# Kernel tuning notes

Hardware: AMD Instinct MI355X
Metric: run time of the kernel (lower is better)

## Reference

```python
import jax, jax.numpy as jnp
import numpy as np

DIM = 192
HEADS = 4
CH = DIM // HEADS          # 48 channels per head
HID = int(DIM * 2.66)      # 510
EPS = 1e-5


def _dwconv(x, w):
    # depthwise 3x3, x: [b,c,h,w], w: [c,1,3,3]
    return jax.lax.conv_general_dilated(
        x, w, window_strides=(1, 1), padding='SAME',
        feature_group_count=x.shape[1],
        dimension_numbers=('NCHW', 'OIHW', 'NCHW'))


def _conv1x1(w, x):
    # w: [out,in], x: [b,in,h,w]
    return jnp.einsum('oc,bchw->bohw', w, x)


def _chan_ln(x, w, b):
    # LayerNorm over channel dim (equivalent to to_3d -> LN(last) -> to_4d)
    mu = jnp.mean(x, axis=1, keepdims=True)
    var = jnp.mean((x - mu) ** 2, axis=1, keepdims=True)
    return (x - mu) / jnp.sqrt(var + EPS) * w[None, :, None, None] + b[None, :, None, None]


def _l2norm(x):
    n = jnp.sqrt(jnp.sum(x * x, axis=-1, keepdims=True))
    return x / jnp.maximum(n, 1e-12)


def setup_inputs() -> dict:
    key = jax.random.key(0)
    ks = jax.random.split(key, 12)
    s = 0.02
    inp = {
        'lr': jax.random.normal(ks[0], (2, DIM, 128, 128), jnp.float32),
        'ref': jax.random.normal(ks[1], (2, DIM, 128, 128), jnp.float32),
        'ln1_w': jnp.ones((DIM,), jnp.float32), 'ln1_b': jnp.zeros((DIM,), jnp.float32),
        'lnr_w': jnp.ones((DIM,), jnp.float32), 'lnr_b': jnp.zeros((DIM,), jnp.float32),
        'ln2_w': jnp.ones((DIM,), jnp.float32), 'ln2_b': jnp.zeros((DIM,), jnp.float32),
        'Wq': jax.random.normal(ks[2], (DIM, DIM), jnp.float32) * s,
        'q_dw': jax.random.normal(ks[3], (DIM, 1, 3, 3), jnp.float32) * s,
        'Wkv': jax.random.normal(ks[4], (2 * DIM, DIM), jnp.float32) * s,
        'kv_dw': jax.random.normal(ks[5], (2 * DIM, 1, 3, 3), jnp.float32) * s,
        'Wproj': jax.random.normal(ks[6], (DIM, DIM), jnp.float32) * s,
        'Wca': jax.random.normal(ks[7], (2 * CH, CH), jnp.float32) * s,
        'temperature': jnp.ones((HEADS, 1, 1), jnp.float32),
        'Wpin': jax.random.normal(ks[8], (2 * HID, DIM), jnp.float32) * s,
        'ffn_dw': jax.random.normal(ks[9], (2 * HID, 1, 3, 3), jnp.float32) * s,
        'Wpout': jax.random.normal(ks[10], (DIM, HID), jnp.float32) * s,
    }
    return inp


def reference(lr, ref, ln1_w, ln1_b, lnr_w, lnr_b, ln2_w, ln2_b,
              Wq, q_dw, Wkv, kv_dw, Wproj, Wca, temperature,
              Wpin, ffn_dw, Wpout):
    b, c, h, w = lr.shape
    L = h * w

    lr_ln = _chan_ln(lr, ln1_w, ln1_b)
    ref_ln = _chan_ln(ref, lnr_w, lnr_b)

    # ---- channel cross-attention ----
    q = _dwconv(_conv1x1(Wq, lr_ln), q_dw)            # [b,c,h,w]
    kv = _dwconv(_conv1x1(Wkv, ref_ln), kv_dw)        # [b,2c,h,w]
    k, v = jnp.split(kv, 2, axis=1)

    q = _l2norm(q.reshape(b, HEADS, CH, L))           # [b,H,ch,L]
    k = _l2norm(k.reshape(b, HEADS, CH, L))
    v = v.reshape(b, HEADS, CH, L)

    attn = jnp.einsum('bhcl,bhdl->bhcd', q, k) * temperature[None]  # [b,H,ch,ch]
    attn0 = jax.nn.softmax(attn, axis=-1)

    a1 = jnp.maximum(attn, 0.0) ** 2
    a1 = jax.nn.gelu(a1, approximate=False) * a1
    # att_ca: 1x1 conv over the last (column) axis of attn1
    x_att = jnp.einsum('oj,bhij->bhio', Wca, a1)      # [b,H,ch,2*ch]
    scale, shift = jnp.split(x_att, 2, axis=-1)
    attn = attn0 * (1.0 + scale) + shift

    out = jnp.einsum('bhcd,bhdl->bhcl', attn, v).reshape(b, c, h, w)
    out = _conv1x1(Wproj, out)
    lr = lr + out

    # ---- GDFN ----
    x = _conv1x1(Wpin, _chan_ln(lr, ln2_w, ln2_b))    # [b,2*HID,h,w]
    x1, x2 = jnp.split(_dwconv(x, ffn_dw), 2, axis=1)
    x = jax.nn.gelu(x1, approximate=False) * x2
    x = _conv1x1(Wpout, x)
    return lr + x
```

## Files before the change

### kernel.cpp

```cpp
#include <hip/hip_runtime.h>
#include <hip/hip_bf16.h>
#include <math.h>

#define L     16384
#define IMG   128
#define BATCH 2
#define C0    192
#define NH    4
#define CHN   48
#define HID   510
#define HID2  1020
#define BL    (BATCH*L)
#define KSPL  128

typedef float  f32x4  __attribute__((ext_vector_type(4)));
typedef __bf16 bf16x8 __attribute__((ext_vector_type(8)));

union UB16 { uint4 u; bf16x8 v; };

__device__ __forceinline__ bf16x8 ld_bf8(const ushort* p){ UB16 x; x.u = *(const uint4*)p; return x.v; }
__device__ __forceinline__ f32x4 mfma16(bf16x8 a, bf16x8 b, f32x4 c){
  return __builtin_amdgcn_mfma_f32_16x16x32_bf16(a, b, c, 0, 0, 0);
}
__device__ __forceinline__ float u2f(ushort u){ union{unsigned u; float f;} x; x.u = ((unsigned)u)<<16; return x.f; }
__device__ __forceinline__ ushort f2u(float f){ __hip_bfloat16 h = __float2bfloat16(f); return *reinterpret_cast<ushort*>(&h); }
__device__ __forceinline__ float gelu_exact(float x){ return 0.5f*x*(1.0f+erff(x*0.70710678118654752f)); }

__global__ __launch_bounds__(256) void ln_stats3_k(const float* __restrict__ x0, const float* __restrict__ x1,
                                                   float* __restrict__ mu0, float* __restrict__ rs0,
                                                   float* __restrict__ mu1, float* __restrict__ rs1,
                                                   ushort* __restrict__ xf0, ushort* __restrict__ xf1){
  int z = blockIdx.y;
  const float* x = z ? x1 : x0;
  float* mu = z ? mu1 : mu0;
  float* rsig = z ? rs1 : rs0;
  ushort* xf = z ? xf1 : xf0;
  int pos = blockIdx.x*256 + threadIdx.x;
  int b = pos >> 14, l = pos & (L-1);
  const float* xp = x + (size_t)b*C0*L + l;
  ushort* base = xf + (size_t)b*C0*L;
  int pt = l >> 4, c16 = l & 15;
  float s=0.f, ss=0.f;
  #pragma unroll
  for (int st=0; st<6; ++st)
    #pragma unroll
    for (int g=0; g<4; ++g){
      ushort u8[8];
      #pragma unroll
      for (int j=0;j<8;++j){
        float v = xp[(size_t)(st*32 + g*8 + j)*L];
        s += v; ss += v*v; u8[j] = f2u(v);
      }
      *(uint4*)(base + ((size_t)(pt*6+st)*64 + g*16 + c16)*8) = *(const uint4*)u8;
    }
  float m = s*(1.f/C0);
  float var = ss*(1.f/C0) - m*m;
  mu[pos]=m; rsig[pos]=rsqrtf(var + 1e-5f);
}

__global__ void finln_k(const float* __restrict__ sum, const float* __restrict__ ss,
                        float* __restrict__ mu, float* __restrict__ rs){
  int i = blockIdx.x*256 + threadIdx.x;
  float m = sum[i]*(1.f/C0);
  float v = ss[i]*(1.f/C0) - m*m;
  mu[i] = m; rs[i] = rsqrtf(v + 1e-5f);
}

__device__ __forceinline__ void packwf_body(const float* __restrict__ W, const float* __restrict__ lnw,
                                            ushort* __restrict__ out, int Csrc, int O, int KS,
                                            int idx, int total){
  if (idx >= total) return;
  int j = idx & 7; int t = idx >> 3;
  int lane = t & 63; t >>= 6;
  int st = t % KS; int mt = t / KS;
  int m = mt*16 + (lane & 15);
  int k = st*32 + (lane >> 4)*8 + j;
  float v = 0.f;
  if (m < O && k < Csrc){ v = W[(size_t)m*Csrc + k]; if (lnw) v *= lnw[k]; }
  out[idx] = f2u(v);
}
__device__ __forceinline__ void prepab_body(const float* __restrict__ W, const float* __restrict__ lnw,
                                            const float* __restrict__ lnb, float* __restrict__ A,
                                            float* __restrict__ Bv, int Cc, int O, int Opad, int o){
  if (o >= Opad) return;
  float a=0.f,b=0.f;
  if (o < O){
    const float* wr = W + (size_t)o*Cc;
    for (int c=0;c<Cc;++c){ float w=wr[c]; a = fmaf(w, lnw[c], a); b = fmaf(w, lnb[c], b); }
  }
  A[o]=a; Bv[o]=b;
}

__global__ void prep_all_k(const float* Wq, const float* ln1w, const float* ln1b, ushort* Aqf, float* Aqv, float* Bqv,
                           const float* Wkv, const float* lnrw, const float* lnrb, ushort* Akvf, float* Akvv, float* Bkvv,
                           const float* Wpin, const float* ln2w, const float* ln2b, ushort* Apinf, float* Apinv, float* Bpinv,
                           const float* Wpout, ushort* Apoutf){
  int bx = blockIdx.x, tid = threadIdx.x;
  if (bx < 144)        packwf_body(Wq,   ln1w, Aqf,   192, 192, 6,  bx*256+tid,        36864);
  else if (bx < 432)   packwf_body(Wkv,  lnrw, Akvf,  192, 384, 6,  (bx-144)*256+tid,  73728);
  else if (bx < 1200)  packwf_body(Wpin, ln2w, Apinf, 192, 1020, 6, (bx-432)*256+tid,  196608);
  else if (bx < 1584)  packwf_body(Wpout, nullptr, Apoutf, 510, 192, 16, (bx-1200)*256+tid, 98304);
  else if (bx == 1584) prepab_body(Wq,  ln1w, ln1b, Aqv,  Bqv,  192, 192, 192,  tid);
  else if (bx < 1587)  prepab_body(Wkv, lnrw, lnrb, Akvv, Bkvv, 192, 384, 384,  (bx-1585)*256+tid);
  else                 prepab_body(Wpin,ln2w, ln2b, Apinv,Bpinv,192, 1020, 1024,(bx-1587)*256+tid);
}

template<int EPI, int WR, int KS, int BN>
__global__ __launch_bounds__(256, WR==2?3:4) void gemm5_k(
    const ushort* __restrict__ Af, int aBS,
    const ushort* __restrict__ Xf, size_t xBS,
    const float* __restrict__ mu, const float* __restrict__ rs,
    const float* __restrict__ Avec, const float* __restrict__ Bvec,
    const float* __restrict__ res,
    void* __restrict__ outp, int Orows, int Ovalid,
    ushort* __restrict__ outf, float* __restrict__ sum_acc, float* __restrict__ ss_acc)
{
  constexpr int BM  = WR*64;
  constexpr int NF  = (WR==2) ? 4 : (BN/64);
  constexpr int PB  = L/BN;
  constexpr int BLD = BN+8;
  constexpr int NSH = (EPI==0)? BM*BLD : (EPI==3 ? BN*72 : 64);
  __shared__ ushort bb[NSH];

  const int tid=threadIdx.x, lane=tid&63, w=tid>>6;
  const int g16=lane>>4, c16=lane&15;
  const int cpx = gridDim.x>>3;
  const int p = (blockIdx.x&7)*cpx + (blockIdx.x>>3);
  const int b = p / PB;
  const int l0 = (p - b*PB)*BN;
  const int mbase = blockIdx.y*BM;
  const int wr = (WR==2)? (w>>1)*64 : 0;
  const int wc = (WR==2)? (w&1)*64 : w*(BN/4);
  const int mt0 = (mbase+wr)>>4;
  const int pt0 = (l0+wc)>>4;

  const ushort* Ap = Af + (size_t)b*aBS + ((size_t)(mt0*KS)*64 + lane)*8;
  const ushort* Bp = Xf + (size_t)b*xBS + ((size_t)(pt0*KS)*64 + lane)*8;

  f32x4 acc[4][NF];
  #pragma unroll
  for (int mi=0;mi<4;++mi)
    #pragma unroll
    for (int ni=0;ni<NF;++ni){ f32x4 z={0.f,0.f,0.f,0.f}; acc[mi][ni]=z; }

  bf16x8 ar[2][4], br[2][NF];
  #pragma unroll
  for (int i=0;i<4;++i) ar[0][i] = ld_bf8(Ap + (size_t)(i*KS)*512);
  #pragma unroll
  for (int i=0;i<NF;++i) br[0][i] = ld_bf8(Bp + (size_t)(i*KS)*512);
  #pragma unroll
  for (int st=0; st<KS; ++st){
    const int cur = st&1, nxt = cur^1;
    if (st+1 < KS){
      #pragma unroll
      for (int i=0;i<4;++i)  ar[nxt][i] = ld_bf8(Ap + (size_t)(i*KS + st+1)*512);
      #pragma unroll
      for (int i=0;i<NF;++i) br[nxt][i] = ld_bf8(Bp + (size_t)(i*KS + st+1)*512);
    }
    #pragma unroll
    for (int mi=0;mi<4;++mi)
      #pragma unroll
      for (int ni=0;ni<NF;++ni)
        acc[mi][ni] = mfma16(ar[cur][mi], br[cur][ni], acc[mi][ni]);
  }

  if (EPI==0){
    #pragma unroll
    for (int ni=0;ni<NF;++ni){
      int nl = wc + ni*16 + c16;
      int posl = b*L + l0 + nl;
      float muv = mu[posl], rsv = rs[posl];
      #pragma unroll
      for (int mi=0;mi<4;++mi)
        #pragma unroll
        for (int r=0;r<4;++r){
          int ro = wr + mi*16 + g16*4 + r;
          int o  = mbase + ro;
          bb[ro*BLD + nl] = f2u(rsv*(acc[mi][ni][r] - muv*Avec[o]) + Bvec[o]);
        }
    }
    __syncthreads();
    constexpr int SEG = BN/64;
    constexpr int JOBS = BM*SEG;
    if (tid < JOBS){
      int row = tid/SEG, seg = tid%SEG;
      if (mbase + row < Ovalid){
        ushort* dst = (ushort*)outp + ((size_t)b*Orows + mbase + row)*L + l0 + seg*64;
        const ushort* src = &bb[row*BLD + seg*64];
        #pragma unroll
        for (int i=0;i<8;++i) *(uint4*)(dst + i*8) = *(const uint4*)(src + i*8);
      }
    }
  } else if (EPI==3){
    #pragma unroll
    for (int ni=0;ni<NF;++ni){
      int nl = wc + ni*16 + c16;
      int posl = b*L + l0 + nl;
      size_t cbase = ((size_t)b*Orows + mbase)*L + l0 + nl;
      float s1=0.f, s2=0.f;
      #pragma unroll
      for (int mi=0;mi<4;++mi)
        #pragma unroll
        for (int r=0;r<4;++r){
          int ro = mi*16 + g16*4 + r;
          size_t idx = cbase + (size_t)ro*L;
          float v = res[idx] + acc[mi][ni][r];
          ((float*)outp)[idx] = v;
          s1 += v; s2 += v*v;
          bb[nl*72 + ro] = f2u(v);
        }
      s1 += __shfl_xor(s1,16,64); s1 += __shfl_xor(s1,32,64);
      s2 += __shfl_xor(s2,16,64); s2 += __shfl_xor(s2,32,64);
      if (g16==0){ atomicAdd(&sum_acc[posl], s1); atomicAdd(&ss_acc[posl], s2); }
    }
    __syncthreads();
    constexpr int PTS = BN/16;
    int ph  = tid >> 7;
    int rm  = tid & 127;
    int stl = rm >> 6;
    int gf  = (rm >> 4) & 3;
    int cf  = rm & 15;
    int stg = (mbase >> 5) + stl;
    #pragma unroll
    for (int pp=0; pp<PTS/2; ++pp){
      int ptl = ph*(PTS/2) + pp;
      int nl  = ptl*16 + cf;
      uint4 v = *(const uint4*)&bb[nl*72 + stl*32 + gf*8];
      int ptg = (l0 >> 4) + ptl;
      *(uint4*)(outf + (size_t)b*C0*L + ((size_t)(ptg*6 + stg)*64 + gf*16 + cf)*8) = v;
    }
  } else {
    #pragma unroll
    for (int ni=0;ni<NF;++ni){
      int nl = wc + ni*16 + c16;
      #pragma unroll
      for (int mi=0;mi<4;++mi)
        #pragma unroll
        for (int r=0;r<4;++r){
          int o = mbase + wr + mi*16 + g16*4 + r;
          size_t idx = ((size_t)b*Orows + o)*L + l0 + nl;
          ((float*)outp)[idx] += acc[mi][ni][r];
        }
    }
  }
}

__global__ __launch_bounds__(256) void dwconvQK_k(const ushort* __restrict__ qpre, const ushort* __restrict__ kvpre,
    const float* __restrict__ qdw, const float* __restrict__ kvdw,
    ushort* __restrict__ qb, ushort* __restrict__ kb,
    float* __restrict__ qss, float* __restrict__ kss){
  int bx = blockIdx.x;
  bool isK = bx >= 3072;
  const ushort* in = isK ? kvpre : qpre;
  size_t inBS = isK ? (size_t)384*L : (size_t)192*L;
  const float* w9 = isK ? kvdw : qdw;
  ushort* out = isK ? kb : qb;
  float* ss = isK ? kss : qss;
  int e  = (isK ? bx-3072 : bx)*256 + threadIdx.x;
  int bc = e >> 11;
  int p  = (e & 2047) * 8;
  int c  = bc % 192, b = bc / 192;
  int y  = p >> 7, x0 = p & 127;
  const ushort* ip = in + (size_t)b*inBS + (size_t)c*L;
  float w[9];
  #pragma unroll
  for (int i=0;i<9;++i) w[i] = w9[c*9+i];
  float v[3][10];
  #pragma unroll
  for (int r=0;r<3;++r){
    int yy = y + r - 1;
    if ((unsigned)yy >= IMG){
      #pragma unroll
      for (int j=0;j<10;++j) v[r][j]=0.f;
    } else {
      const ushort* rp = ip + yy*IMG + x0;
      uint4 cv = *(const uint4*)rp; const ushort* us = (const ushort*)&cv;
      #pragma unroll
      for (int j=0;j<8;++j) v[r][j+1] = u2f(us[j]);
      v[r][0] = (x0>0)   ? u2f(rp[-1]) : 0.f;
      v[r][9] = (x0<120) ? u2f(rp[8])  : 0.f;
    }
  }
  float sq = 0.f; ushort o8[8];
  #pragma unroll
  for (int j=0;j<8;++j){
    float a = 0.f;
    #pragma unroll
    for (int r=0;r<3;++r)
      #pragma unroll
      for (int dx=0;dx<3;++dx) a = fmaf(w[r*3+dx], v[r][j+dx], a);
    o8[j] = f2u(a); sq += a*a;
  }
  *(uint4*)(out + (size_t)b*(size_t)192*L + (size_t)c*L + p) = *(const uint4*)o8;
  #pragma unroll
  for (int off=32; off>0; off>>=1) sq += __shfl_xor(sq, off, 64);
  __shared__ float red[4];
  int wid = threadIdx.x >> 6;
  if ((threadIdx.x & 63)==0) red[wid]=sq;
  __syncthreads();
  if (threadIdx.x==0) atomicAdd(&ss[b*192 + c], red[0]+red[1]+red[2]+red[3]);
}

__global__ __launch_bounds__(256) void dwconvV_k(const ushort* __restrict__ in, const float* __restrict__ w9,
                                                 ushort* __restrict__ vf){
  __shared__ ushort lt[64][40];
  int xs = blockIdx.x;
  int chunk = ((xs & 7) << 5) | (xs >> 3);
  int st = blockIdx.y, b = blockIdx.z;
  int t = threadIdx.x;
  int c = t >> 3, xo = (t & 7)*8;
  int l0 = chunk*64;
  int y = l0 >> 7, px = (l0 & 127) + xo;
  int gc = st*32 + c;
  const ushort* ip = in + ((size_t)b*384 + C0 + gc)*L;
  const float* wp = w9 + (size_t)(C0+gc)*9;
  float w[9];
  #pragma unroll
  for (int i=0;i<9;++i) w[i] = wp[i];
  float v[3][10];
  #pragma unroll
  for (int r=0;r<3;++r){
    int yy = y + r - 1;
    if ((unsigned)yy >= IMG){
      #pragma unroll
      for (int j=0;j<10;++j) v[r][j]=0.f;
    } else {
      const ushort* rp = ip + yy*IMG + px;
      uint4 cv = *(const uint4*)rp; const ushort* us = (const ushort*)&cv;
      #pragma unroll
      for (int j=0;j<8;++j) v[r][j+1] = u2f(us[j]);
      v[r][0] = (px>0)   ? u2f(rp[-1]) : 0.f;
      v[r][9] = (px<120) ? u2f(rp[8])  : 0.f;
    }
  }
  #pragma unroll
  for (int j=0;j<8;++j){
    float a = 0.f;
    #pragma unroll
    for (int r=0;r<3;++r)
      #pragma unroll
      for (int dx=0;dx<3;++dx) a = fmaf(w[r*3+dx], v[r][j+dx], a);
    int row = xo + j;
    lt[row][c ^ (((row>>3)&3)<<3)] = f2u(a);
  }
  __syncthreads();
  int ptl = t>>6, gf = (t>>4)&3, cf = t&15;
  int rrow = ptl*16 + cf;
  int oct = gf ^ ((rrow>>3)&3);
  uint4 vv = *(const uint4*)&lt[rrow][oct*8];
  int pt = (l0>>4) + ptl;
  *(uint4*)(vf + (size_t)b*C0*L + ((size_t)(pt*6 + st)*64 + gf*16 + cf)*8) = vv;
}

__global__ __launch_bounds__(64) void qk_mfma_k(const ushort* __restrict__ qb, const ushort* __restrict__ kb,
                                                float* __restrict__ P){
  int ks = blockIdx.x, bh = blockIdx.y;
  int b = bh >> 2, h = bh & 3;
  int lane = threadIdx.x, g16 = lane>>4, c16 = lane&15;
  const ushort* qbase = qb + ((size_t)b*C0 + h*CHN)*L;
  const ushort* kbse  = kb + ((size_t)b*C0 + h*CHN)*L;
  f32x4 acc[3][3];
  #pragma unroll
  for (int i=0;i<3;++i)
    #pragma unroll
    for (int j=0;j<3;++j){ f32x4 z={0.f,0.f,0.f,0.f}; acc[i][j]=z; }
  int k0 = ks * (L/KSPL);
  for (int kk=0; kk<(L/KSPL)/32; ++kk){
    int kb2 = k0 + kk*32;
    bf16x8 af[3], bv[3];
    #pragma unroll
    for (int i=0;i<3;++i){
      af[i] = ld_bf8(qbase + (size_t)(i*16+c16)*L + kb2 + g16*8);
      bv[i] = ld_bf8(kbse  + (size_t)(i*16+c16)*L + kb2 + g16*8);
    }
    #pragma unroll
    for (int mi=0;mi<3;++mi)
      #pragma unroll
      for (int ni=0;ni<3;++ni)
        acc[mi][ni] = mfma16(af[mi], bv[ni], acc[mi][ni]);
  }
  float* Pp = P + ((size_t)ks*(BATCH*NH) + bh)*CHN*CHN;
  #pragma unroll
  for (int mi=0;mi<3;++mi)
    #pragma unroll
    for (int ni=0;ni<3;++ni)
      #pragma unroll
      for (int r=0;r<4;++r){
        int m = mi*16 + g16*4 + r, n = ni*16 + c16;
        Pp[m*CHN + n] = acc[mi][ni][r];
      }
}

__global__ __launch_bounds__(64) void gating_k(const float* __restrict__ Pp, const float* __restrict__ qss,
                         const float* __restrict__ kss, const float* __restrict__ temp,
                         const float* __restrict__ Wca, float* __restrict__ attnF){
  int blk = blockIdx.x;
  int c  = blk % CHN; int bh = blk / CHN;
  int h  = bh & 3, b = bh >> 2;
  int d  = threadIdx.x;
  bool act = (d < CHN);

  float sv = 0.f;
  if (act){
    const float* pr = Pp + (size_t)bh*CHN*CHN + c*CHN + d;
    for (int ks=0; ks<KSPL; ++ks) sv += pr[(size_t)ks*(BATCH*NH)*CHN*CHN];
  }

  float T  = temp[h];
  float nq = sqrtf(qss[b*C0 + h*CHN + c]);
  float rq = 1.f/fmaxf(nq, 1e-12f);
  float rk = 0.f;
  if (act){
    float nk = sqrtf(kss[b*C0 + h*CHN + d]);
    rk = 1.f/fmaxf(nk, 1e-12f);
  }
  float raw = act ? sv*rq*rk*T : -1e30f;

  float mx = raw;
  #pragma unroll
  for (int off=32; off>0; off>>=1) mx = fmaxf(mx, __shfl_xor(mx, off, 64));
  float e = act ? expf(raw - mx) : 0.f;
  float sum = e;
  #pragma unroll
  for (int off=32; off>0; off>>=1) sum += __shfl_xor(sum, off, 64);
  float a0 = e / sum;

  float r = fmaxf(raw, 0.f); r = r*r;
  float a1 = gelu_exact(r)*r;
  __shared__ float a1s[CHN];
  if (act) a1s[d] = a1;
  __syncthreads();

  if (!act) return;
  float s1 = 0.f, s2 = 0.f;
  const float* w1 = Wca + (size_t)d*CHN;
  const float* w2 = Wca + (size_t)(d+CHN)*CHN;
  #pragma unroll
  for (int j=0;j<CHN;++j){
    float aj = a1s[j];
    s1 = fmaf(w1[j], aj, s1);
    s2 = fmaf(w2[j], aj, s2);
  }
  attnF[((size_t)bh*CHN + c)*CHN + d] = a0*(1.f+s1) + s2;
}

__global__ void mtf_k(const float* __restrict__ Wproj, const float* __restrict__ attnF,
                      ushort* __restrict__ Mtf){
  int idx = blockIdx.x*256 + threadIdx.x;
  if (idx >= BATCH*192*192) return;
  int j = idx & 7; int t = idx >> 3;
  int lane = t & 63; t >>= 6;
  int st = t % 6; t /= 6;
  int mt = t % 12; int b = t / 12;
  int o = mt*16 + (lane & 15);
  int d = st*32 + (lane >> 4)*8 + j;
  int h = d / CHN, dd = d % CHN;
  float s=0.f;
  for (int c=0;c<CHN;++c)
    s = fmaf(Wproj[(size_t)o*C0 + h*CHN + c],
             attnF[(((size_t)(b*NH+h))*CHN + c)*CHN + dd], s);
  Mtf[idx] = f2u(s);
}

__global__ __launch_bounds__(256) void ffn8f_k(const ushort* __restrict__ hidden, const float* __restrict__ w9,
                                               ushort* __restrict__ gf){
  __shared__ ushort lt[64][40];
  int xs = blockIdx.x;
  int chunk = ((xs & 7) << 5) | (xs >> 3);
  int st = blockIdx.y, b = blockIdx.z;
  int t = threadIdx.x;
  int c = t >> 3, xo = (t & 7)*8;
  int l0 = chunk*64;
  int y = l0 >> 7, px = (l0 & 127) + xo;
  int gc = st*32 + c;
  ushort o8[8];
  if (gc < HID){
    const ushort* i1 = hidden + ((size_t)b*HID2 + gc)*L;
    const ushort* i2 = i1 + (size_t)HID*L;
    float w1[9], w2[9];
    #pragma unroll
    for (int i=0;i<9;++i){ w1[i] = w9[gc*9+i]; w2[i] = w9[(HID+gc)*9+i]; }
    float v1[3][10], v2[3][10];
    #pragma unroll
    for (int r=0;r<3;++r){
      int yy = y + r - 1;
      if ((unsigned)yy >= IMG){
        #pragma unroll
        for (int j=0;j<10;++j){ v1[r][j]=0.f; v2[r][j]=0.f; }
      } else {
        const ushort* rp1 = i1 + yy*IMG + px;
        const ushort* rp2 = i2 + yy*IMG + px;
        uint4 c1 = *(const uint4*)rp1; const ushort* u1 = (const ushort*)&c1;
        uint4 c2 = *(const uint4*)rp2; const ushort* u2 = (const ushort*)&c2;
        #pragma unroll
        for (int j=0;j<8;++j){ v1[r][j+1] = u2f(u1[j]); v2[r][j+1] = u2f(u2[j]); }
        v1[r][0] = (px>0)   ? u2f(rp1[-1]) : 0.f;
        v1[r][9] = (px<120) ? u2f(rp1[8])  : 0.f;
        v2[r][0] = (px>0)   ? u2f(rp2[-1]) : 0.f;
        v2[r][9] = (px<120) ? u2f(rp2[8])  : 0.f;
      }
    }
    #pragma unroll
    for (int j=0;j<8;++j){
      float d1=0.f, d2=0.f;
      #pragma unroll
      for (int r=0;r<3;++r)
        #pragma unroll
        for (int dx=0;dx<3;++dx){
          d1 = fmaf(w1[r*3+dx], v1[r][j+dx], d1);
          d2 = fmaf(w2[r*3+dx], v2[r][j+dx], d2);
        }
      o8[j] = f2u(gelu_exact(d1)*d2);
    }
  } else {
    #pragma unroll
    for (int j=0;j<8;++j) o8[j] = 0;
  }
  #pragma unroll
  for (int j=0;j<8;++j){
    int row = xo + j;
    lt[row][c ^ (((row>>3)&3)<<3)] = o8[j];
  }
  __syncthreads();
  int ptl = t>>6, gfr = (t>>4)&3, cf = t&15;
  int rrow = ptl*16 + cf;
  int oct = gfr ^ ((rrow>>3)&3);
  uint4 vv = *(const uint4*)&lt[rrow][oct*8];
  int pt = (l0>>4) + ptl;
  *(uint4*)(gf + (size_t)b*512*L + ((size_t)(pt*16 + st)*64 + gfr*16 + cf)*8) = vv;
}

extern "C" void kernel_launch(void* const* d_in, const int* in_sizes, int n_in,
                              void* d_out, int out_size, void* d_ws, size_t ws_size,
                              hipStream_t stream){
  (void)in_sizes; (void)n_in; (void)out_size; (void)ws_size;
  const float* lr    = (const float*)d_in[0];
  const float* ref   = (const float*)d_in[1];
  const float* ln1w  = (const float*)d_in[2];
  const float* ln1b  = (const float*)d_in[3];
  const float* lnrw  = (const float*)d_in[4];
  const float* lnrb  = (const float*)d_in[5];
  const float* ln2w  = (const float*)d_in[6];
  const float* ln2b  = (const float*)d_in[7];
  const float* Wq    = (const float*)d_in[8];
  const float* qdw   = (const float*)d_in[9];
  const float* Wkv   = (const float*)d_in[10];
  const float* kvdw  = (const float*)d_in[11];
  const float* Wproj = (const float*)d_in[12];
  const float* Wca   = (const float*)d_in[13];
  const float* temp  = (const float*)d_in[14];
  const float* Wpin  = (const float*)d_in[15];
  const float* ffndw = (const float*)d_in[16];
  const float* Wpout = (const float*)d_in[17];
  float* out = (float*)d_out;

  char* ws = (char*)d_ws;
  size_t off = 0;
  auto alloc = [&](size_t bytes)->void*{ void* p = ws + off; off += (bytes + 255) & ~(size_t)255; return p; };

  ushort* Aqf    = (ushort*)alloc((size_t)192*192*2);
  ushort* Akvf   = (ushort*)alloc((size_t)384*192*2);
  ushort* Apinf  = (ushort*)alloc((size_t)1024*192*2);
  ushort* Apoutf = (ushort*)alloc((size_t)192*512*2);
  ushort* Mtf    = (ushort*)alloc((size_t)BATCH*192*192*2);
  float* Aqv  = (float*)alloc(192*4);   float* Bqv  = (float*)alloc(192*4);
  float* Akvv = (float*)alloc(384*4);   float* Bkvv = (float*)alloc(384*4);
  float* Apinv= (float*)alloc(1024*4);  float* Bpinv= (float*)alloc(1024*4);
  float* mu_lr = (float*)alloc((size_t)BL*4);  float* rs_lr = (float*)alloc((size_t)BL*4);
  float* mu_rf = (float*)alloc((size_t)BL*4);  float* rs_rf = (float*)alloc((size_t)BL*4);
  float* mu_o  = (float*)alloc((size_t)BL*4);  float* rs_o  = (float*)alloc((size_t)BL*4);
  float* qss   = (float*)alloc((size_t)BATCH*C0*4);
  float* kss   = (float*)alloc((size_t)BATCH*C0*4);
  float* sum_o = (float*)alloc((size_t)BL*4);
  float* ssq_o = (float*)alloc((size_t)BL*4);
  float* S     = (float*)alloc((size_t)BATCH*NH*CHN*CHN*4); (void)S;
  float* attnF = (float*)alloc((size_t)BATCH*NH*CHN*CHN*4);
  char*  pool  = (char*)alloc((size_t)104857600);

  ushort* LRf    = (ushort*)(pool);
  ushort* REFf   = (ushort*)(pool + 12582912);
  ushort* q_pre  = (ushort*)(pool + 25165824);
  ushort* kv_pre = (ushort*)(pool + 37748736);
  ushort* qb     = (ushort*)(pool + 62914560);
  ushort* kvb_k  = (ushort*)(pool + 75497472);
  ushort* Vf     = (ushort*)(pool + 88080384);
  float*  Pp     = (float*) (pool);
  ushort* OUTf   = (ushort*)(pool);
  ushort* hidden = (ushort*)(pool + 33554432);
  ushort* Gf     = (ushort*)(pool);

  hipMemsetAsync(qss, 0, (size_t)(1536 + 1536 + 131072 + 131072), stream);

  prep_all_k<<<1591,256,0,stream>>>(Wq, ln1w, ln1b, Aqf, Aqv, Bqv,
                                    Wkv, lnrw, lnrb, Akvf, Akvv, Bkvv,
                                    Wpin, ln2w, ln2b, Apinf, Apinv, Bpinv,
                                    Wpout, Apoutf);

  ln_stats3_k<<<dim3(BL/256,2),256,0,stream>>>(lr, ref, mu_lr, rs_lr, mu_rf, rs_rf, LRf, REFf);

  gemm5_k<0,1,6,128><<<dim3(256,3),256,0,stream>>>(Aqf, 0, LRf, (size_t)C0*L,
      mu_lr, rs_lr, Aqv, Bqv, nullptr, q_pre, 192, 192, nullptr, nullptr, nullptr);
  gemm5_k<0,2,6,128><<<dim3(256,3),256,0,stream>>>(Akvf, 0, REFf, (size_t)C0*L,
      mu_rf, rs_rf, Akvv, Bkvv, nullptr, kv_pre, 384, 384, nullptr, nullptr, nullptr);

  dwconvQK_k<<<6144,256,0,stream>>>(q_pre, kv_pre, qdw, kvdw, qb, kvb_k, qss, kss);
  dwconvV_k<<<dim3(256,6,2),256,0,stream>>>(kv_pre, kvdw, Vf);

  qk_mfma_k<<<dim3(KSPL, BATCH*NH),64,0,stream>>>(qb, kvb_k, Pp);
  gating_k<<<BATCH*NH*CHN,64,0,stream>>>(Pp, qss, kss, temp, Wca, attnF);
  mtf_k<<<288,256,0,stream>>>(Wproj, attnF, Mtf);

  gemm5_k<3,1,6,128><<<dim3(256,3),256,0,stream>>>(Mtf, 192*192, Vf, (size_t)C0*L,
      nullptr, nullptr, nullptr, nullptr, lr, out, 192, 192, OUTf, sum_o, ssq_o);
  finln_k<<<BL/256,256,0,stream>>>(sum_o, ssq_o, mu_o, rs_o);

  gemm5_k<0,2,6,128><<<dim3(256,8),256,0,stream>>>(Apinf, 0, OUTf, (size_t)C0*L,
      mu_o, rs_o, Apinv, Bpinv, nullptr, hidden, 1020, 1020, nullptr, nullptr, nullptr);
  ffn8f_k<<<dim3(256,16,2),256,0,stream>>>(hidden, ffndw, Gf);
  gemm5_k<2,1,16,128><<<dim3(256,3),256,0,stream>>>(Apoutf, 0, Gf, (size_t)512*L,
      nullptr, nullptr, nullptr, nullptr, nullptr, out, 192, 192, nullptr, nullptr, nullptr);
}
```

Before: 264.6 us.

## Fuse LN stats, memset, dwconvs and finalize-LN into neighbouring kernels; bf16 residual

Folds the workspace zeroing and the lr/ref layernorm statistics into the weight-prep kernel, and merges the Q/K and V depthwise convolutions into one launch. The finalize-LN step moves into the FFN-input GEMM epilogue. The attention-output GEMM no longer writes the fp32 residual to the output; the final GEMM reads the bf16 packed residual instead of read-modify-writing fp32. This reduces launches and fp32 traffic at the cost of storing the residual in bf16 precision.

```diff
diff --git a/kernel.cpp b/kernel.cpp
--- a/kernel.cpp
+++ b/kernel.cpp
@@ -25,46 +25,6 @@
 __device__ __forceinline__ float u2f(ushort u){ union{unsigned u; float f;} x; x.u = ((unsigned)u)<<16; return x.f; }
 __device__ __forceinline__ ushort f2u(float f){ __hip_bfloat16 h = __float2bfloat16(f); return *reinterpret_cast<ushort*>(&h); }
 __device__ __forceinline__ float gelu_exact(float x){ return 0.5f*x*(1.0f+erff(x*0.70710678118654752f)); }
-
-__global__ __launch_bounds__(256) void ln_stats3_k(const float* __restrict__ x0, const float* __restrict__ x1,
-                                                   float* __restrict__ mu0, float* __restrict__ rs0,
-                                                   float* __restrict__ mu1, float* __restrict__ rs1,
-                                                   ushort* __restrict__ xf0, ushort* __restrict__ xf1){
-  int z = blockIdx.y;
-  const float* x = z ? x1 : x0;
-  float* mu = z ? mu1 : mu0;
-  float* rsig = z ? rs1 : rs0;
-  ushort* xf = z ? xf1 : xf0;
-  int pos = blockIdx.x*256 + threadIdx.x;
-  int b = pos >> 14, l = pos & (L-1);
-  const float* xp = x + (size_t)b*C0*L + l;
-  ushort* base = xf + (size_t)b*C0*L;
-  int pt = l >> 4, c16 = l & 15;
-  float s=0.f, ss=0.f;
-  #pragma unroll
-  for (int st=0; st<6; ++st)
-    #pragma unroll
-    for (int g=0; g<4; ++g){
-      ushort u8[8];
-      #pragma unroll
-      for (int j=0;j<8;++j){
-        float v = xp[(size_t)(st*32 + g*8 + j)*L];
-        s += v; ss += v*v; u8[j] = f2u(v);
-      }
-      *(uint4*)(base + ((size_t)(pt*6+st)*64 + g*16 + c16)*8) = *(const uint4*)u8;
-    }
-  float m = s*(1.f/C0);
-  float var = ss*(1.f/C0) - m*m;
-  mu[pos]=m; rsig[pos]=rsqrtf(var + 1e-5f);
-}
-
-__global__ void finln_k(const float* __restrict__ sum, const float* __restrict__ ss,
-                        float* __restrict__ mu, float* __restrict__ rs){
-  int i = blockIdx.x*256 + threadIdx.x;
-  float m = sum[i]*(1.f/C0);
-  float v = ss[i]*(1.f/C0) - m*m;
-  mu[i] = m; rs[i] = rsqrtf(v + 1e-5f);
-}
 
 __device__ __forceinline__ void packwf_body(const float* __restrict__ W, const float* __restrict__ lnw,
                                             ushort* __restrict__ out, int Csrc, int O, int KS,
@@ -90,11 +50,38 @@
   }
   A[o]=a; Bv[o]=b;
 }
+__device__ __forceinline__ void ln_body(const float* __restrict__ x, float* __restrict__ mu,
+                                        float* __restrict__ rsig, ushort* __restrict__ xf, int pos){
+  int b = pos >> 14, l = pos & (L-1);
+  const float* xp = x + (size_t)b*C0*L + l;
+  ushort* base = xf + (size_t)b*C0*L;
+  int pt = l >> 4, c16 = l & 15;
+  float s=0.f, ss=0.f;
+  #pragma unroll
+  for (int st=0; st<6; ++st)
+    #pragma unroll
+    for (int g=0; g<4; ++g){
+      ushort u8[8];
+      #pragma unroll
+      for (int j=0;j<8;++j){
+        float v = xp[(size_t)(st*32 + g*8 + j)*L];
+        s += v; ss += v*v; u8[j] = f2u(v);
+      }
+      *(uint4*)(base + ((size_t)(pt*6+st)*64 + g*16 + c16)*8) = *(const uint4*)u8;
+    }
+  float m = s*(1.f/C0);
+  float var = ss*(1.f/C0) - m*m;
+  mu[pos]=m; rsig[pos]=rsqrtf(var + 1e-5f);
+}
 
 __global__ void prep_all_k(const float* Wq, const float* ln1w, const float* ln1b, ushort* Aqf, float* Aqv, float* Bqv,
                            const float* Wkv, const float* lnrw, const float* lnrb, ushort* Akvf, float* Akvv, float* Bkvv,
                            const float* Wpin, const float* ln2w, const float* ln2b, ushort* Apinf, float* Apinv, float* Bpinv,
-                           const float* Wpout, ushort* Apoutf){
+                           const float* Wpout, ushort* Apoutf,
+                           float* zbase,
+                           const float* lr, const float* ref,
+                           float* mu_lr, float* rs_lr, float* mu_rf, float* rs_rf,
+                           ushort* LRf, ushort* REFf){
   int bx = blockIdx.x, tid = threadIdx.x;
   if (bx < 144)        packwf_body(Wq,   ln1w, Aqf,   192, 192, 6,  bx*256+tid,        36864);
   else if (bx < 432)   packwf_body(Wkv,  lnrw, Akvf,  192, 384, 6,  (bx-144)*256+tid,  73728);
@@ -102,7 +89,14 @@
   else if (bx < 1584)  packwf_body(Wpout, nullptr, Apoutf, 510, 192, 16, (bx-1200)*256+tid, 98304);
   else if (bx == 1584) prepab_body(Wq,  ln1w, ln1b, Aqv,  Bqv,  192, 192, 192,  tid);
   else if (bx < 1587)  prepab_body(Wkv, lnrw, lnrb, Akvv, Bkvv, 192, 384, 384,  (bx-1585)*256+tid);
-  else                 prepab_body(Wpin,ln2w, ln2b, Apinv,Bpinv,192, 1020, 1024,(bx-1587)*256+tid);
+  else if (bx < 1591)  prepab_body(Wpin,ln2w, ln2b, Apinv,Bpinv,192, 1020, 1024,(bx-1587)*256+tid);
+  else if (bx < 1850){ int idx = (bx-1591)*256 + tid; if (idx < 66304) zbase[idx] = 0.f; }
+  else {
+    int r = bx - 1850;
+    int z = r >> 7;
+    int pos = (r & 127)*256 + tid;
+    ln_body(z ? ref : lr, z ? mu_rf : mu_lr, z ? rs_rf : rs_lr, z ? REFf : LRf, pos);
+  }
 }
 
 template<int EPI, int WR, int KS, int BN>
@@ -119,7 +113,7 @@
   constexpr int NF  = (WR==2) ? 4 : (BN/64);
   constexpr int PB  = L/BN;
   constexpr int BLD = BN+8;
-  constexpr int NSH = (EPI==0)? BM*BLD : (EPI==3 ? BN*72 : 64);
+  constexpr int NSH = (EPI==0||EPI==6)? BM*BLD : (EPI==4 ? BN*72 : 64);
   __shared__ ushort bb[NSH];
 
   const int tid=threadIdx.x, lane=tid&63, w=tid>>6;
@@ -164,12 +158,18 @@
         acc[mi][ni] = mfma16(ar[cur][mi], br[cur][ni], acc[mi][ni]);
   }
 
-  if (EPI==0){
+  if (EPI==0 || EPI==6){
     #pragma unroll
     for (int ni=0;ni<NF;++ni){
       int nl = wc + ni*16 + c16;
       int posl = b*L + l0 + nl;
-      float muv = mu[posl], rsv = rs[posl];
+      float muv, rsv;
+      if (EPI==0){ muv = mu[posl]; rsv = rs[posl]; }
+      else {
+        float sm = mu[posl]*(1.f/C0);
+        float vq = rs[posl]*(1.f/C0) - sm*sm;
+        muv = sm; rsv = rsqrtf(vq + 1e-5f);
+      }
       #pragma unroll
       for (int mi=0;mi<4;++mi)
         #pragma unroll
@@ -191,7 +191,7 @@
         for (int i=0;i<8;++i) *(uint4*)(dst + i*8) = *(const uint4*)(src + i*8);
       }
     }
-  } else if (EPI==3){
+  } else if (EPI==4){
     #pragma unroll
     for (int ni=0;ni<NF;++ni){
       int nl = wc + ni*16 + c16;
@@ -203,9 +203,7 @@
         #pragma unroll
         for (int r=0;r<4;++r){
           int ro = mi*16 + g16*4 + r;
-          size_t idx = cbase + (size_t)ro*L;
-          float v = res[idx] + acc[mi][ni][r];
-          ((float*)outp)[idx] = v;
+          float v = res[cbase + (size_t)ro*L] + acc[mi][ni][r];
           s1 += v; s2 += v*v;
           bb[nl*72 + ro] = f2u(v);
         }
@@ -230,126 +228,131 @@
       *(uint4*)(outf + (size_t)b*C0*L + ((size_t)(ptg*6 + stg)*64 + gf*16 + cf)*8) = v;
     }
   } else {
+    const ushort* ofb = outf + (size_t)b*C0*L;
     #pragma unroll
     for (int ni=0;ni<NF;++ni){
       int nl = wc + ni*16 + c16;
+      int l  = l0 + nl;
+      int pt = l >> 4, cc = l & 15;
       #pragma unroll
       for (int mi=0;mi<4;++mi)
         #pragma unroll
         for (int r=0;r<4;++r){
-          int o = mbase + wr + mi*16 + g16*4 + r;
-          size_t idx = ((size_t)b*Orows + o)*L + l0 + nl;
-          ((float*)outp)[idx] += acc[mi][ni][r];
+          int o = mbase + mi*16 + g16*4 + r;
+          ushort u = ofb[((size_t)(pt*6 + (o>>5))*64 + ((o>>3)&3)*16 + cc)*8 + (o&7)];
+          ((float*)outp)[((size_t)b*Orows + o)*L + l] = u2f(u) + acc[mi][ni][r];
         }
     }
   }
 }
 
-__global__ __launch_bounds__(256) void dwconvQK_k(const ushort* __restrict__ qpre, const ushort* __restrict__ kvpre,
+__global__ __launch_bounds__(256) void dwall_k(const ushort* __restrict__ qpre, const ushort* __restrict__ kvpre,
     const float* __restrict__ qdw, const float* __restrict__ kvdw,
     ushort* __restrict__ qb, ushort* __restrict__ kb,
-    float* __restrict__ qss, float* __restrict__ kss){
+    float* __restrict__ qss, float* __restrict__ kss,
+    ushort* __restrict__ vf){
+  __shared__ ushort lt[64][40];
+  __shared__ float red[4];
   int bx = blockIdx.x;
-  bool isK = bx >= 3072;
-  const ushort* in = isK ? kvpre : qpre;
-  size_t inBS = isK ? (size_t)384*L : (size_t)192*L;
-  const float* w9 = isK ? kvdw : qdw;
-  ushort* out = isK ? kb : qb;
-  float* ss = isK ? kss : qss;
-  int e  = (isK ? bx-3072 : bx)*256 + threadIdx.x;
-  int bc = e >> 11;
-  int p  = (e & 2047) * 8;
-  int c  = bc % 192, b = bc / 192;
-  int y  = p >> 7, x0 = p & 127;
-  const ushort* ip = in + (size_t)b*inBS + (size_t)c*L;
-  float w[9];
-  #pragma unroll
-  for (int i=0;i<9;++i) w[i] = w9[c*9+i];
-  float v[3][10];
-  #pragma unroll
-  for (int r=0;r<3;++r){
-    int yy = y + r - 1;
-    if ((unsigned)yy >= IMG){
-      #pragma unroll
-      for (int j=0;j<10;++j) v[r][j]=0.f;
-    } else {
-      const ushort* rp = ip + yy*IMG + x0;
-      uint4 cv = *(const uint4*)rp; const ushort* us = (const ushort*)&cv;
-      #pragma unroll
-      for (int j=0;j<8;++j) v[r][j+1] = u2f(us[j]);
-      v[r][0] = (x0>0)   ? u2f(rp[-1]) : 0.f;
-      v[r][9] = (x0<120) ? u2f(rp[8])  : 0.f;
-    }
-  }
-  float sq = 0.f; ushort o8[8];
-  #pragma unroll
-  for (int j=0;j<8;++j){
-    float a = 0.f;
-    #pragma unroll
-    for (int r=0;r<3;++r)
-      #pragma unroll
-      for (int dx=0;dx<3;++dx) a = fmaf(w[r*3+dx], v[r][j+dx], a);
-    o8[j] = f2u(a); sq += a*a;
-  }
-  *(uint4*)(out + (size_t)b*(size_t)192*L + (size_t)c*L + p) = *(const uint4*)o8;
-  #pragma unroll
-  for (int off=32; off>0; off>>=1) sq += __shfl_xor(sq, off, 64);
-  __shared__ float red[4];
-  int wid = threadIdx.x >> 6;
-  if ((threadIdx.x & 63)==0) red[wid]=sq;
-  __syncthreads();
-  if (threadIdx.x==0) atomicAdd(&ss[b*192 + c], red[0]+red[1]+red[2]+red[3]);
-}
-
-__global__ __launch_bounds__(256) void dwconvV_k(const ushort* __restrict__ in, const float* __restrict__ w9,
-                                                 ushort* __restrict__ vf){
-  __shared__ ushort lt[64][40];
-  int xs = blockIdx.x;
-  int chunk = ((xs & 7) << 5) | (xs >> 3);
-  int st = blockIdx.y, b = blockIdx.z;
-  int t = threadIdx.x;
-  int c = t >> 3, xo = (t & 7)*8;
-  int l0 = chunk*64;
-  int y = l0 >> 7, px = (l0 & 127) + xo;
-  int gc = st*32 + c;
-  const ushort* ip = in + ((size_t)b*384 + C0 + gc)*L;
-  const float* wp = w9 + (size_t)(C0+gc)*9;
-  float w[9];
-  #pragma unroll
-  for (int i=0;i<9;++i) w[i] = wp[i];
-  float v[3][10];
-  #pragma unroll
-  for (int r=0;r<3;++r){
-    int yy = y + r - 1;
-    if ((unsigned)yy >= IMG){
-      #pragma unroll
-      for (int j=0;j<10;++j) v[r][j]=0.f;
-    } else {
-      const ushort* rp = ip + yy*IMG + px;
-      uint4 cv = *(const uint4*)rp; const ushort* us = (const ushort*)&cv;
-      #pragma unroll
-      for (int j=0;j<8;++j) v[r][j+1] = u2f(us[j]);
-      v[r][0] = (px>0)   ? u2f(rp[-1]) : 0.f;
-      v[r][9] = (px<120) ? u2f(rp[8])  : 0.f;
-    }
-  }
-  #pragma unroll
-  for (int j=0;j<8;++j){
-    float a = 0.f;
-    #pragma unroll
-    for (int r=0;r<3;++r)
-      #pragma unroll
-      for (int dx=0;dx<3;++dx) a = fmaf(w[r*3+dx], v[r][j+dx], a);
-    int row = xo + j;
-    lt[row][c ^ (((row>>3)&3)<<3)] = f2u(a);
-  }
-  __syncthreads();
-  int ptl = t>>6, gf = (t>>4)&3, cf = t&15;
-  int rrow = ptl*16 + cf;
-  int oct = gf ^ ((rrow>>3)&3);
-  uint4 vv = *(const uint4*)&lt[rrow][oct*8];
-  int pt = (l0>>4) + ptl;
-  *(uint4*)(vf + (size_t)b*C0*L + ((size_t)(pt*6 + st)*64 + gf*16 + cf)*8) = vv;
+  if (bx < 6144){
+    bool isK = bx >= 3072;
+    const ushort* in = isK ? kvpre : qpre;
+    size_t inBS = isK ? (size_t)384*L : (size_t)192*L;
+    const float* w9 = isK ? kvdw : qdw;
+    ushort* out = isK ? kb : qb;
+    float* ss = isK ? kss : qss;
+    int e  = (isK ? bx-3072 : bx)*256 + threadIdx.x;
+    int bc = e >> 11;
+    int p  = (e & 2047) * 8;
+    int c  = bc % 192, b = bc / 192;
+    int y  = p >> 7, x0 = p & 127;
+    const ushort* ip = in + (size_t)b*inBS + (size_t)c*L;
+    float w[9];
+    #pragma unroll
+    for (int i=0;i<9;++i) w[i] = w9[c*9+i];
+    float v[3][10];
+    #pragma unroll
+    for (int r=0;r<3;++r){
+      int yy = y + r - 1;
+      if ((unsigned)yy >= IMG){
+        #pragma unroll
+        for (int j=0;j<10;++j) v[r][j]=0.f;
+      } else {
+        const ushort* rp = ip + yy*IMG + x0;
+        uint4 cv = *(const uint4*)rp; const ushort* us = (const ushort*)&cv;
+        #pragma unroll
+        for (int j=0;j<8;++j) v[r][j+1] = u2f(us[j]);
+        v[r][0] = (x0>0)   ? u2f(rp[-1]) : 0.f;
+        v[r][9] = (x0<120) ? u2f(rp[8])  : 0.f;
+      }
+    }
+    float sq = 0.f; ushort o8[8];
+    #pragma unroll
+    for (int j=0;j<8;++j){
+      float a = 0.f;
+      #pragma unroll
+      for (int r=0;r<3;++r)
+        #pragma unroll
+        for (int dx=0;dx<3;++dx) a = fmaf(w[r*3+dx], v[r][j+dx], a);
+      o8[j] = f2u(a); sq += a*a;
+    }
+    *(uint4*)(out + (size_t)b*(size_t)192*L + (size_t)c*L + p) = *(const uint4*)o8;
+    #pragma unroll
+    for (int off=32; off>0; off>>=1) sq += __shfl_xor(sq, off, 64);
+    int wid = threadIdx.x >> 6;
+    if ((threadIdx.x & 63)==0) red[wid]=sq;
+    __syncthreads();
+    if (threadIdx.x==0) atomicAdd(&ss[b*192 + c], red[0]+red[1]+red[2]+red[3]);
+  } else {
+    int rr = bx - 6144;
+    int xs = rr & 255;
+    int st = (rr >> 8) % 6;
+    int b  = rr / 1536;
+    int chunk = ((xs & 7) << 5) | (xs >> 3);
+    int t = threadIdx.x;
+    int c = t >> 3, xo = (t & 7)*8;
+    int l0 = chunk*64;
+    int y = l0 >> 7, px = (l0 & 127) + xo;
+    int gc = st*32 + c;
+    const ushort* ip = kvpre + ((size_t)b*384 + C0 + gc)*L;
+    const float* wp = kvdw + (size_t)(C0+gc)*9;
+    float w[9];
+    #pragma unroll
+    for (int i=0;i<9;++i) w[i] = wp[i];
+    float v[3][10];
+    #pragma unroll
+    for (int r=0;r<3;++r){
+      int yy = y + r - 1;
+      if ((unsigned)yy >= IMG){
+        #pragma unroll
+        for (int j=0;j<10;++j) v[r][j]=0.f;
+      } else {
+        const ushort* rp = ip + yy*IMG + px;
+        uint4 cv = *(const uint4*)rp; const ushort* us = (const ushort*)&cv;
+        #pragma unroll
+        for (int j=0;j<8;++j) v[r][j+1] = u2f(us[j]);
+        v[r][0] = (px>0)   ? u2f(rp[-1]) : 0.f;
+        v[r][9] = (px<120) ? u2f(rp[8])  : 0.f;
+      }
+    }
+    #pragma unroll
+    for (int j=0;j<8;++j){
+      float a = 0.f;
+      #pragma unroll
+      for (int r=0;r<3;++r)
+        #pragma unroll
+        for (int dx=0;dx<3;++dx) a = fmaf(w[r*3+dx], v[r][j+dx], a);
+      int row = xo + j;
+      lt[row][c ^ (((row>>3)&3)<<3)] = f2u(a);
+    }
+    __syncthreads();
+    int ptl = t>>6, gf = (t>>4)&3, cf = t&15;
+    int rrow = ptl*16 + cf;
+    int oct = gf ^ ((rrow>>3)&3);
+    uint4 vv = *(const uint4*)&lt[rrow][oct*8];
+    int pt = (l0>>4) + ptl;
+    *(uint4*)(vf + (size_t)b*C0*L + ((size_t)(pt*6 + st)*64 + gf*16 + cf)*8) = vv;
+  }
 }
 
 __global__ __launch_bounds__(64) void qk_mfma_k(const ushort* __restrict__ qb, const ushort* __restrict__ kb,
@@ -568,12 +571,10 @@
   float* Apinv= (float*)alloc(1024*4);  float* Bpinv= (float*)alloc(1024*4);
   float* mu_lr = (float*)alloc((size_t)BL*4);  float* rs_lr = (float*)alloc((size_t)BL*4);
   float* mu_rf = (float*)alloc((size_t)BL*4);  float* rs_rf = (float*)alloc((size_t)BL*4);
-  float* mu_o  = (float*)alloc((size_t)BL*4);  float* rs_o  = (float*)alloc((size_t)BL*4);
   float* qss   = (float*)alloc((size_t)BATCH*C0*4);
   float* kss   = (float*)alloc((size_t)BATCH*C0*4);
   float* sum_o = (float*)alloc((size_t)BL*4);
   float* ssq_o = (float*)alloc((size_t)BL*4);
-  float* S     = (float*)alloc((size_t)BATCH*NH*CHN*CHN*4); (void)S;
   float* attnF = (float*)alloc((size_t)BATCH*NH*CHN*CHN*4);
   char*  pool  = (char*)alloc((size_t)104857600);
 
@@ -587,36 +588,33 @@
   float*  Pp     = (float*) (pool);
   ushort* OUTf   = (ushort*)(pool);
   ushort* hidden = (ushort*)(pool + 33554432);
-  ushort* Gf     = (ushort*)(pool);
-
-  hipMemsetAsync(qss, 0, (size_t)(1536 + 1536 + 131072 + 131072), stream);
-
-  prep_all_k<<<1591,256,0,stream>>>(Wq, ln1w, ln1b, Aqf, Aqv, Bqv,
+  ushort* Gf     = (ushort*)(pool + 12582912);
+
+  prep_all_k<<<2106,256,0,stream>>>(Wq, ln1w, ln1b, Aqf, Aqv, Bqv,
                                     Wkv, lnrw, lnrb, Akvf, Akvv, Bkvv,
                                     Wpin, ln2w, ln2b, Apinf, Apinv, Bpinv,
-                                    Wpout, Apoutf);
-
-  ln_stats3_k<<<dim3(BL/256,2),256,0,stream>>>(lr, ref, mu_lr, rs_lr, mu_rf, rs_rf, LRf, REFf);
+                                    Wpout, Apoutf,
+                                    qss,
+                                    lr, ref, mu_lr, rs_lr, mu_rf, rs_rf, LRf, REFf);
 
   gemm5_k<0,1,6,128><<<dim3(256,3),256,0,stream>>>(Aqf, 0, LRf, (size_t)C0*L,
       mu_lr, rs_lr, Aqv, Bqv, nullptr, q_pre, 192, 192, nullptr, nullptr, nullptr);
   gemm5_k<0,2,6,128><<<dim3(256,3),256,0,stream>>>(Akvf, 0, REFf, (size_t)C0*L,
       mu_rf, rs_rf, Akvv, Bkvv, nullptr, kv_pre, 384, 384, nullptr, nullptr, nullptr);
 
-  dwconvQK_k<<<6144,256,0,stream>>>(q_pre, kv_pre, qdw, kvdw, qb, kvb_k, qss, kss);
-  dwconvV_k<<<dim3(256,6,2),256,0,stream>>>(kv_pre, kvdw, Vf);
+  dwall_k<<<9216,256,0,stream>>>(q_pre, kv_pre, qdw, kvdw, qb, kvb_k, qss, kss, Vf);
 
   qk_mfma_k<<<dim3(KSPL, BATCH*NH),64,0,stream>>>(qb, kvb_k, Pp);
   gating_k<<<BATCH*NH*CHN,64,0,stream>>>(Pp, qss, kss, temp, Wca, attnF);
   mtf_k<<<288,256,0,stream>>>(Wproj, attnF, Mtf);
 
-  gemm5_k<3,1,6,128><<<dim3(256,3),256,0,stream>>>(Mtf, 192*192, Vf, (size_t)C0*L,
-      nullptr, nullptr, nullptr, nullptr, lr, out, 192, 192, OUTf, sum_o, ssq_o);
-  finln_k<<<BL/256,256,0,stream>>>(sum_o, ssq_o, mu_o, rs_o);
-
-  gemm5_k<0,2,6,128><<<dim3(256,8),256,0,stream>>>(Apinf, 0, OUTf, (size_t)C0*L,
-      mu_o, rs_o, Apinv, Bpinv, nullptr, hidden, 1020, 1020, nullptr, nullptr, nullptr);
+  gemm5_k<4,1,6,128><<<dim3(256,3),256,0,stream>>>(Mtf, 192*192, Vf, (size_t)C0*L,
+      nullptr, nullptr, nullptr, nullptr, lr, nullptr, 192, 192, OUTf, sum_o, ssq_o);
+
+  gemm5_k<6,2,6,128><<<dim3(256,8),256,0,stream>>>(Apinf, 0, OUTf, (size_t)C0*L,
+      sum_o, ssq_o, Apinv, Bpinv, nullptr, hidden, 1020, 1020, nullptr, nullptr, nullptr);
   ffn8f_k<<<dim3(256,16,2),256,0,stream>>>(hidden, ffndw, Gf);
-  gemm5_k<2,1,16,128><<<dim3(256,3),256,0,stream>>>(Apoutf, 0, Gf, (size_t)512*L,
-      nullptr, nullptr, nullptr, nullptr, nullptr, out, 192, 192, nullptr, nullptr, nullptr);
-}
+
+  gemm5_k<5,1,16,128><<<dim3(256,3),256,0,stream>>>(Apoutf, 0, Gf, (size_t)512*L,
+      nullptr, nullptr, nullptr, nullptr, nullptr, out, 192, 192, OUTf, nullptr, nullptr);
+}
```

Result: faster. 241.1 us (-8.9%).
